# Performance work log

Measured on AMD Instinct MI355X. Metric: run time of the kernel, lower is better.

Reference implementation:

```python
import jax, jax.numpy as jnp
import numpy as np

B, N, C = 8, 1024, 768
H = 12
HD = C // H  # 64
SCALE = C ** (-0.5)  # NOTE: source scales by n_emb^-0.5, not head_dim^-0.5


def setup_inputs() -> dict:
    key = jax.random.key(0)
    k1, k2, k3 = jax.random.split(key, 3)
    x = jax.random.normal(k1, (B, N, C), dtype=jnp.float32)
    W_qkv = jax.random.normal(k2, (C, 3 * C), dtype=jnp.float32) * (C ** -0.5)
    b_qkv = jnp.zeros((3 * C,), dtype=jnp.float32)
    W_proj = jax.random.normal(k3, (C, C), dtype=jnp.float32) * (C ** -0.5)
    b_proj = jnp.zeros((C,), dtype=jnp.float32)
    return {"x": x, "W_qkv": W_qkv, "b_qkv": b_qkv, "W_proj": W_proj, "b_proj": b_proj}


def reference(x, W_qkv, b_qkv, W_proj, b_proj):
    # qkv projection: (B,N,3C) -> (3,B,H,N,HD)
    qkv = x @ W_qkv + b_qkv
    qkv = qkv.reshape(B, N, 3, H, HD).transpose(2, 0, 3, 1, 4)
    q, k, v = qkv[0], qkv[1], qkv[2]
    # scaled dot-product attention (full N x N, as in source)
    attn = jnp.einsum("bhnd,bhmd->bhnm", q, k) * SCALE
    attn = jax.nn.softmax(attn, axis=-1)
    out = jnp.einsum("bhnm,bhmd->bhnd", attn, v)
    out = out.transpose(0, 2, 1, 3).reshape(B, N, C)
    return out @ W_proj + b_proj
```

## Files before the change

kernel.cpp:

```cpp
#include <hip/hip_runtime.h>
#include <hip/hip_bf16.h>
#include <stdint.h>

#define Bb 8
#define Nn_ 1024
#define Cc_ 768
#define Hh 12
#define HDd 64
#define BHh 96
#define SCALE_F 0.03608439182435161f
#define CL2F (0.03608439182435161f * 1.4426950408889634f)
#define THRRAW (3.0f / CL2F)

typedef __attribute__((ext_vector_type(4))) float f32x4;
typedef __attribute__((ext_vector_type(8))) __bf16 bf16x8;

__device__ __forceinline__ unsigned short f2bf(float f) {
  uint32_t u = __builtin_bit_cast(uint32_t, f);
  uint32_t r = (u + 0x7fffu + ((u >> 16) & 1u)) >> 16;
  return (unsigned short)r;
}

__device__ __forceinline__ uint32_t cvtpk(float a, float b) {
  uint32_t r;
  asm("v_cvt_pk_bf16_f32 %0, %1, %2" : "=v"(r) : "v"(a), "v"(b));
  return r;
}

__device__ __forceinline__ f32x4 mfma16(bf16x8 a, bf16x8 b, f32x4 c) {
  return __builtin_amdgcn_mfma_f32_16x16x32_bf16(a, b, c, 0, 0, 0);
}

typedef const __attribute__((address_space(1))) uint32_t* gas1_t;
typedef __attribute__((address_space(3))) uint32_t* las3_t;
__device__ __forceinline__ void gl_lds16(const void* g, void* l) {
  __builtin_amdgcn_global_load_lds((gas1_t)g, (las3_t)l, 16, 0, 0);
}

#define VMCNT(n) asm volatile("s_waitcnt vmcnt(" #n ")" ::: "memory")
#define SBAR() __builtin_amdgcn_s_barrier()
#define SCHED_FENCE() __builtin_amdgcn_sched_barrier(0)

__global__ void k_cvt_x(const float* __restrict__ x, unsigned short* __restrict__ xb, int n4) {
  int i = blockIdx.x * blockDim.x + threadIdx.x;
  if (i >= n4) return;
  float4 v = ((const float4*)x)[i];
  ushort4 o;
  o.x = f2bf(v.x); o.y = f2bf(v.y); o.z = f2bf(v.z); o.w = f2bf(v.w);
  ((ushort4*)xb)[i] = o;
}

template <int R, int CC>
__global__ void k_transpose(const float* __restrict__ src, unsigned short* __restrict__ dst) {
  __shared__ unsigned short tile[64][65];
  int c0 = blockIdx.x * 64;
  int r0 = blockIdx.y * 64;
  int t = threadIdx.x;
#pragma unroll
  for (int i = 0; i < 16; ++i) {
    int idx = t + 256 * i;
    int r = idx >> 6, c = idx & 63;
    tile[r][c] = f2bf(src[(size_t)(r0 + r) * CC + c0 + c]);
  }
  __syncthreads();
#pragma unroll
  for (int i = 0; i < 16; ++i) {
    int idx = t + 256 * i;
    int a = idx >> 6, bq = idx & 63;
    dst[(size_t)(c0 + a) * R + r0 + bq] = tile[bq][a];
  }
}

__global__ __launch_bounds__(256) void k_transpose_v(const unsigned short* __restrict__ V,
                                                     unsigned short* __restrict__ Vt) {
  __shared__ unsigned short tile[64][72];
  int bh = blockIdx.y;
  int n0 = blockIdx.x * 64;
  int t = threadIdx.x;
  const unsigned short* src = V + ((size_t)bh * 1024 + n0) * 64;
#pragma unroll
  for (int i = 0; i < 4; ++i) {
    int idx = t + i * 256;
    int r = idx >> 4, c4 = idx & 15;
    ushort4 v = ((const ushort4*)src)[idx];
    tile[r][c4 * 4 + 0] = v.x; tile[r][c4 * 4 + 1] = v.y;
    tile[r][c4 * 4 + 2] = v.z; tile[r][c4 * 4 + 3] = v.w;
  }
  __syncthreads();
  unsigned short* dst = Vt + (size_t)bh * 64 * 1024 + n0;
#pragma unroll
  for (int i = 0; i < 4; ++i) {
    int idx = t + i * 256;
    int c = idx >> 4, n4 = idx & 15;
    ushort4 o;
    o.x = tile[n4 * 4 + 0][c]; o.y = tile[n4 * 4 + 1][c];
    o.z = tile[n4 * 4 + 2][c]; o.w = tile[n4 * 4 + 3][c];
    ((ushort4*)(dst + (size_t)c * 1024))[n4] = o;
  }
}

#define BM 128
#define BN 128

template <int EPI>
__global__ __launch_bounds__(256, 2) void k_gemm(
    const unsigned short* __restrict__ A, const unsigned short* __restrict__ Bt,
    const float* __restrict__ bias, float* __restrict__ out,
    unsigned short* __restrict__ Qb, unsigned short* __restrict__ Kb,
    unsigned short* __restrict__ Vb, int M, int Nw) {
  __shared__ char smem[2][32768];
  int t = threadIdx.x;
  int w = t >> 6, lane = t & 63;
  int g = lane >> 4, l15 = lane & 15;
  int m0 = blockIdx.x * BM;
  int n0 = blockIdx.y * BN;
  int wr = w >> 1, wc = w & 1;

  f32x4 acc[4][4] = {};

  int soff[4];
  const char* gA[4];
  const char* gB[4];
#pragma unroll
  for (int it = 0; it < 4; ++it) {
    int off = it * 4096 + t * 16;
    soff[it] = it * 4096 + w * 1024;
    int row = off >> 7;
    int sb = (off & 127) ^ ((row & 7) << 4);
    gA[it] = (const char*)A + (size_t)(m0 + row) * 1536 + sb;
    gB[it] = (const char*)Bt + (size_t)(n0 + row) * 1536 + sb;
  }

  auto STG = [&](int buf, int kt) {
    char* As = smem[buf];
    char* Bs = smem[buf] + 16384;
#pragma unroll
    for (int it = 0; it < 4; ++it) gl_lds16(gA[it] + kt * 128, As + soff[it]);
#pragma unroll
    for (int it = 0; it < 4; ++it) gl_lds16(gB[it] + kt * 128, Bs + soff[it]);
  };

  const char *pa[2][4], *pb[2][4];
#pragma unroll
  for (int ks = 0; ks < 2; ++ks) {
    int kb = ks * 64 + g * 16;
#pragma unroll
    for (int mi = 0; mi < 4; ++mi) {
      int rowA = wr * 64 + mi * 16 + l15;
      pa[ks][mi] = smem[0] + rowA * 128 + (kb ^ ((rowA & 7) << 4));
      int rowB = wc * 64 + mi * 16 + l15;
      pb[ks][mi] = smem[0] + 16384 + rowB * 128 + (kb ^ ((rowB & 7) << 4));
    }
  }

  auto CMP = [&](int off) {
    bf16x8 av[2][4], bv[2][4];
#pragma unroll
    for (int ks = 0; ks < 2; ++ks)
#pragma unroll
      for (int mi = 0; mi < 4; ++mi) {
        av[ks][mi] = *(const bf16x8*)(pa[ks][mi] + off);
        bv[ks][mi] = *(const bf16x8*)(pb[ks][mi] + off);
      }
#pragma unroll
    for (int ks = 0; ks < 2; ++ks)
#pragma unroll
      for (int mi = 0; mi < 4; ++mi)
#pragma unroll
        for (int ni = 0; ni < 4; ++ni)
          acc[mi][ni] = mfma16(av[ks][mi], bv[ks][ni], acc[mi][ni]);
  };

  STG(0, 0);
#pragma unroll
  for (int kt = 0; kt < 12; ++kt) {
    int cur = kt & 1;
    if (kt < 11) {
      STG(cur ^ 1, kt + 1);
      VMCNT(8);
    } else {
      VMCNT(0);
    }
    SBAR();
    SCHED_FENCE();
    CMP(cur * 32768);
    SCHED_FENCE();
    if (kt < 11) SBAR();
  }

#pragma unroll
  for (int mi = 0; mi < 4; ++mi) {
#pragma unroll
    for (int ni = 0; ni < 4; ++ni) {
      int col = n0 + wc * 64 + ni * 16 + l15;
      float bvs = bias[col];
#pragma unroll
      for (int j = 0; j < 4; ++j) {
        int row = m0 + wr * 64 + mi * 16 + g * 4 + j;
        float val = acc[mi][ni][j] + bvs;
        if constexpr (EPI == 0) {
          out[(size_t)row * Nw + col] = val;
        } else {
          int bI = row >> 10, n = row & 1023;
          int typ = col / 768, within = col % 768;
          int h = within >> 6, d = within & 63;
          int bh = bI * 12 + h;
          unsigned short bf = f2bf(val);
          unsigned short* dst = (typ == 0) ? Qb : (typ == 1) ? Kb : Vb;
          dst[((size_t)bh * 1024 + n) * 64 + d] = bf;
        }
      }
    }
  }
}

__global__ __launch_bounds__(256, 3) void k_attn(
    const unsigned short* __restrict__ Q, const unsigned short* __restrict__ K,
    const unsigned short* __restrict__ Vt, unsigned short* __restrict__ Oa) {
  __shared__ char smem[49152];
  char* Ks = smem;
  char* Ps = smem + 32768;
  int t = threadIdx.x, w = t >> 6, lane = t & 63;
  int g = lane >> 4, l15 = lane & 15;

  int fb = blockIdx.x;
  int bh = (fb & 7) * 12 + ((fb >> 3) % 12);
  int n0 = (fb / 96) * 128;
  int bI = bh / 12, h = bh % 12;
  char* Pw = Ps + w * 4096;

  bf16x8 qf[2][2];
  {
    const char* qbase = (const char*)Q + ((size_t)bh * 1024 + n0 + w * 32 + l15) * 128 + g * 16;
    qf[0][0] = *(const bf16x8*)(qbase);
    qf[0][1] = *(const bf16x8*)(qbase + 64);
    qf[1][0] = *(const bf16x8*)(qbase + 16 * 128);
    qf[1][1] = *(const bf16x8*)(qbase + 16 * 128 + 64);
  }

  f32x4 acc[2][4] = {};
  float mrun[2] = {-INFINITY, -INFINITY};
  float lrun[2] = {0.f, 0.f};

  const char* pK[2][4];
#pragma unroll
  for (int ks = 0; ks < 2; ++ks)
#pragma unroll
    for (int ff = 0; ff < 4; ++ff) {
      int row = ff * 16 + l15;
      pK[ks][ff] = Ks + row * 128 + ((ks * 64 + g * 16) ^ ((row & 7) << 4));
    }
  char* pPw[2][4];
  const char* pPr[2][2];
#pragma unroll
  for (int q = 0; q < 2; ++q) {
    int prow = q * 16 + l15, swz = (l15 & 7) << 4;
#pragma unroll
    for (int ff = 0; ff < 4; ++ff) pPw[q][ff] = Pw + prow * 128 + ((ff * 32 + g * 8) ^ swz);
#pragma unroll
    for (int ks = 0; ks < 2; ++ks) pPr[q][ks] = Pw + prow * 128 + ((ks * 64 + g * 16) ^ swz);
  }

  int o0 = t * 16, o1 = t * 16 + 4096;
  int r0 = o0 >> 7, r1 = o1 >> 7;
  int sb0 = (o0 & 127) ^ ((r0 & 7) << 4);
  int sb1 = (o1 & 127) ^ ((r1 & 7) << 4);
  const char* KgA = (const char*)K + (size_t)bh * 131072 + (size_t)r0 * 128 + sb0;
  const char* KgB = (const char*)K + (size_t)bh * 131072 + (size_t)r1 * 128 + sb1;
  const char* VgA = (const char*)Vt + (size_t)bh * 131072 + (size_t)r0 * 2048 + sb0;
  const char* VgB = (const char*)Vt + (size_t)bh * 131072 + (size_t)r1 * 2048 + sb1;

  auto STG = [&](int buf, int mt) {
    char* Kd = Ks + buf * 8192;
    char* Vd = Ks + 16384 + buf * 8192;
    gl_lds16(KgA + (size_t)mt * 8192, Kd + w * 1024);
    gl_lds16(KgB + (size_t)mt * 8192, Kd + 4096 + w * 1024);
    gl_lds16(VgA + (size_t)mt * 128, Vd + w * 1024);
    gl_lds16(VgB + (size_t)mt * 128, Vd + 4096 + w * 1024);
  };

  auto TILE = [&](int off) {
    f32x4 s[4][2] = {};
#pragma unroll
    for (int ks = 0; ks < 2; ++ks)
#pragma unroll
      for (int ff = 0; ff < 4; ++ff) {
        bf16x8 kv = *(const bf16x8*)(pK[ks][ff] + off);
        s[ff][0] = mfma16(kv, qf[0][ks], s[ff][0]);
        s[ff][1] = mfma16(kv, qf[1][ks], s[ff][1]);
      }

    float pmax[2];
#pragma unroll
    for (int q = 0; q < 2; ++q) {
      float a0 = fmaxf(fmaxf(s[0][q][0], s[0][q][1]), fmaxf(s[0][q][2], s[0][q][3]));
      float a1 = fmaxf(fmaxf(s[1][q][0], s[1][q][1]), fmaxf(s[1][q][2], s[1][q][3]));
      float a2 = fmaxf(fmaxf(s[2][q][0], s[2][q][1]), fmaxf(s[2][q][2], s[2][q][3]));
      float a3 = fmaxf(fmaxf(s[3][q][0], s[3][q][1]), fmaxf(s[3][q][2], s[3][q][3]));
      float pm = fmaxf(fmaxf(a0, a1), fmaxf(a2, a3));
      pm = fmaxf(pm, __shfl_xor(pm, 16, 64));
      pm = fmaxf(pm, __shfl_xor(pm, 32, 64));
      pmax[q] = pm;
    }

    bool upd = (pmax[0] > mrun[0] + THRRAW) || (pmax[1] > mrun[1] + THRRAW);
    if (__any(upd)) {
#pragma unroll
      for (int q = 0; q < 2; ++q) {
        float mnew = fmaxf(mrun[q], pmax[q]);
        float alpha = __builtin_amdgcn_exp2f((mrun[q] - mnew) * CL2F);
        mrun[q] = mnew;
        lrun[q] *= alpha;
#pragma unroll
        for (int j = 0; j < 4; ++j) {
          float aj = __shfl(alpha, g * 4 + j, 64);
          acc[q][0][j] *= aj; acc[q][1][j] *= aj;
          acc[q][2][j] *= aj; acc[q][3][j] *= aj;
        }
      }
    }

#pragma unroll
    for (int q = 0; q < 2; ++q) {
      float nm = -mrun[q] * CL2F;
      float rs = 0.f;
#pragma unroll
      for (int ff = 0; ff < 4; ++ff) {
        float p0 = __builtin_amdgcn_exp2f(fmaf(s[ff][q][0], CL2F, nm));
        float p1 = __builtin_amdgcn_exp2f(fmaf(s[ff][q][1], CL2F, nm));
        float p2 = __builtin_amdgcn_exp2f(fmaf(s[ff][q][2], CL2F, nm));
        float p3 = __builtin_amdgcn_exp2f(fmaf(s[ff][q][3], CL2F, nm));
        rs += (p0 + p1) + (p2 + p3);
        uint2 pk;
        pk.x = cvtpk(p0, p1);
        pk.y = cvtpk(p2, p3);
        *(uint2*)(pPw[q][ff]) = pk;
      }
      rs += __shfl_xor(rs, 16, 64);
      rs += __shfl_xor(rs, 32, 64);
      lrun[q] += rs;
    }

#pragma unroll
    for (int ks = 0; ks < 2; ++ks) {
      bf16x8 pa0 = *(const bf16x8*)(pPr[0][ks]);
      bf16x8 pa1 = *(const bf16x8*)(pPr[1][ks]);
#pragma unroll
      for (int fd = 0; fd < 4; ++fd) {
        bf16x8 vv = *(const bf16x8*)(pK[ks][fd] + 16384 + off);
        acc[0][fd] = mfma16(pa0, vv, acc[0][fd]);
        acc[1][fd] = mfma16(pa1, vv, acc[1][fd]);
      }
    }
  };

  STG(0, 0);
  for (int mt2 = 0; mt2 < 8; ++mt2) {
    STG(1, 2 * mt2 + 1);
    VMCNT(4);
    SBAR();
    SCHED_FENCE();
    TILE(0);
    SCHED_FENCE();
    SBAR();
    if (mt2 < 7) {
      STG(0, 2 * mt2 + 2);
      VMCNT(4);
    } else {
      VMCNT(0);
    }
    SBAR();
    SCHED_FENCE();
    TILE(8192);
    SCHED_FENCE();
    if (mt2 < 7) SBAR();
  }

#pragma unroll
  for (int q = 0; q < 2; ++q) {
#pragma unroll
    for (int j = 0; j < 4; ++j) {
      float lv = __shfl(lrun[q], g * 4 + j, 64);
      float inv = 1.0f / lv;
      int n = n0 + w * 32 + q * 16 + g * 4 + j;
      size_t rowb = ((size_t)bI * 1024 + n) * 768 + h * 64;
#pragma unroll
      for (int fd = 0; fd < 4; ++fd)
        Oa[rowb + fd * 16 + l15] = (unsigned short)(cvtpk(acc[q][fd][j] * inv, 0.f) & 0xffffu);
    }
  }
}

extern "C" void kernel_launch(void* const* d_in, const int* in_sizes, int n_in,
                              void* d_out, int out_size, void* d_ws, size_t ws_size,
                              hipStream_t stream) {
  const float* x = (const float*)d_in[0];
  const float* Wqkv = (const float*)d_in[1];
  const float* bqkv = (const float*)d_in[2];
  const float* Wproj = (const float*)d_in[3];
  const float* bproj = (const float*)d_in[4];
  float* out = (float*)d_out;

  char* ws = (char*)d_ws;
  unsigned short* xb  = (unsigned short*)(ws);
  unsigned short* wqt = (unsigned short*)(ws + 12582912);
  unsigned short* wpt = (unsigned short*)(ws + 16121856);
  unsigned short* Qb  = (unsigned short*)(ws + 17301504);
  unsigned short* Kb  = (unsigned short*)(ws + 29884416);
  unsigned short* Vtb = (unsigned short*)(ws + 42467328);
  unsigned short* Oa  = (unsigned short*)(ws + 55050240);
  unsigned short* Vb  = Oa;

  k_cvt_x<<<dim3(6144), dim3(256), 0, stream>>>(x, xb, (Bb * Nn_ * Cc_) / 4);
  k_transpose<768, 2304><<<dim3(36, 12), dim3(256), 0, stream>>>(Wqkv, wqt);
  k_transpose<768, 768><<<dim3(12, 12), dim3(256), 0, stream>>>(Wproj, wpt);
  k_gemm<1><<<dim3(64, 18), dim3(256), 0, stream>>>(xb, wqt, bqkv, nullptr, Qb, Kb, Vb,
                                                    8192, 2304);
  k_transpose_v<<<dim3(16, 96), dim3(256), 0, stream>>>(Vb, Vtb);
  k_attn<<<dim3(768), dim3(256), 0, stream>>>(Qb, Kb, Vtb, Oa);
  k_gemm<0><<<dim3(64, 6), dim3(256), 0, stream>>>(Oa, wpt, bproj, out, nullptr, nullptr, nullptr,
                                                   8192, 768);
}
```

Measured before the change: 114.1 us.

## Shrink GEMM K-tile, template M-tile, and cut attention LDS and reductions

The GEMM kernel switches from a 128-wide K step with XOR swizzle to a 64-wide K step without swizzle. The M tile becomes a template parameter, so the output projection uses 64-row tiles and launches twice as many blocks, and launch bounds rise to 4 blocks per CU. The attention kernel halves its per-wave P scratch by processing one query group at a time, which cuts LDS to 40KB for higher occupancy. It also defers the row-sum cross-lane reduction to the end, skips the max shuffle unless a rescale is needed, and adds setprio around the MFMA sections. Dropping the swizzle risks LDS bank conflicts, and the smaller K step doubles the number of barriers per GEMM.

```diff
diff --git a/kernel.cpp b/kernel.cpp
--- a/kernel.cpp
+++ b/kernel.cpp
@@ -99,104 +99,95 @@
   }
 }
 
-#define BM 128
-#define BN 128
-
-template <int EPI>
-__global__ __launch_bounds__(256, 2) void k_gemm(
+template <int EPI, int BMt>
+__global__ __launch_bounds__(256, 4) void k_gemm(
     const unsigned short* __restrict__ A, const unsigned short* __restrict__ Bt,
     const float* __restrict__ bias, float* __restrict__ out,
     unsigned short* __restrict__ Qb, unsigned short* __restrict__ Kb,
-    unsigned short* __restrict__ Vb, int M, int Nw) {
-  __shared__ char smem[2][32768];
+    unsigned short* __restrict__ Vb, int Nw) {
+  constexpr int WM = BMt / 2;
+  constexpr int MR = BMt / 32;
+  constexpr int AL = BMt / 64;
+  constexpr int BUFSZ = BMt * 64 + 8192;
+  constexpr int NLD = AL + 2;
+  __shared__ char smem[2 * BUFSZ];
   int t = threadIdx.x;
   int w = t >> 6, lane = t & 63;
   int g = lane >> 4, l15 = lane & 15;
-  int m0 = blockIdx.x * BM;
-  int n0 = blockIdx.y * BN;
+  int m0 = blockIdx.x * BMt;
+  int n0 = blockIdx.y * 128;
   int wr = w >> 1, wc = w & 1;
 
-  f32x4 acc[4][4] = {};
-
-  int soff[4];
-  const char* gA[4];
-  const char* gB[4];
-#pragma unroll
-  for (int it = 0; it < 4; ++it) {
-    int off = it * 4096 + t * 16;
-    soff[it] = it * 4096 + w * 1024;
-    int row = off >> 7;
-    int sb = (off & 127) ^ ((row & 7) << 4);
-    gA[it] = (const char*)A + (size_t)(m0 + row) * 1536 + sb;
-    gB[it] = (const char*)Bt + (size_t)(n0 + row) * 1536 + sb;
+  f32x4 acc[MR][4] = {};
+
+  const char* gA[AL];
+  const char* gB[2];
+  int sA[AL], sB[2];
+#pragma unroll
+  for (int it = 0; it < AL; ++it) {
+    int o = it * 4096 + t * 16;
+    gA[it] = (const char*)A + (size_t)(m0 + (o >> 6)) * 1536 + (o & 63);
+    sA[it] = it * 4096 + w * 1024;
+  }
+#pragma unroll
+  for (int it = 0; it < 2; ++it) {
+    int o = it * 4096 + t * 16;
+    gB[it] = (const char*)Bt + (size_t)(n0 + (o >> 6)) * 1536 + (o & 63);
+    sB[it] = BMt * 64 + it * 4096 + w * 1024;
   }
 
   auto STG = [&](int buf, int kt) {
-    char* As = smem[buf];
-    char* Bs = smem[buf] + 16384;
-#pragma unroll
-    for (int it = 0; it < 4; ++it) gl_lds16(gA[it] + kt * 128, As + soff[it]);
-#pragma unroll
-    for (int it = 0; it < 4; ++it) gl_lds16(gB[it] + kt * 128, Bs + soff[it]);
+    char* base = smem + buf * BUFSZ;
+#pragma unroll
+    for (int it = 0; it < AL; ++it) gl_lds16(gA[it] + kt * 64, base + sA[it]);
+#pragma unroll
+    for (int it = 0; it < 2; ++it) gl_lds16(gB[it] + kt * 64, base + sB[it]);
   };
 
-  const char *pa[2][4], *pb[2][4];
-#pragma unroll
-  for (int ks = 0; ks < 2; ++ks) {
-    int kb = ks * 64 + g * 16;
-#pragma unroll
-    for (int mi = 0; mi < 4; ++mi) {
-      int rowA = wr * 64 + mi * 16 + l15;
-      pa[ks][mi] = smem[0] + rowA * 128 + (kb ^ ((rowA & 7) << 4));
-      int rowB = wc * 64 + mi * 16 + l15;
-      pb[ks][mi] = smem[0] + 16384 + rowB * 128 + (kb ^ ((rowB & 7) << 4));
-    }
-  }
-
-  auto CMP = [&](int off) {
-    bf16x8 av[2][4], bv[2][4];
-#pragma unroll
-    for (int ks = 0; ks < 2; ++ks)
-#pragma unroll
-      for (int mi = 0; mi < 4; ++mi) {
-        av[ks][mi] = *(const bf16x8*)(pa[ks][mi] + off);
-        bv[ks][mi] = *(const bf16x8*)(pb[ks][mi] + off);
-      }
-#pragma unroll
-    for (int ks = 0; ks < 2; ++ks)
-#pragma unroll
-      for (int mi = 0; mi < 4; ++mi)
-#pragma unroll
-        for (int ni = 0; ni < 4; ++ni)
-          acc[mi][ni] = mfma16(av[ks][mi], bv[ks][ni], acc[mi][ni]);
-  };
+  const char* pa[MR];
+  const char* pb[4];
+#pragma unroll
+  for (int mi = 0; mi < MR; ++mi)
+    pa[mi] = smem + (wr * WM + mi * 16 + l15) * 64 + g * 16;
+#pragma unroll
+  for (int ni = 0; ni < 4; ++ni)
+    pb[ni] = smem + BMt * 64 + (wc * 64 + ni * 16 + l15) * 64 + g * 16;
 
   STG(0, 0);
 #pragma unroll
-  for (int kt = 0; kt < 12; ++kt) {
-    int cur = kt & 1;
-    if (kt < 11) {
-      STG(cur ^ 1, kt + 1);
-      VMCNT(8);
+  for (int kt = 0; kt < 24; ++kt) {
+    int off = (kt & 1) * BUFSZ;
+    if (kt < 23) {
+      STG((kt & 1) ^ 1, kt + 1);
+      if constexpr (NLD == 4) { VMCNT(4); } else { VMCNT(3); }
     } else {
       VMCNT(0);
     }
     SBAR();
     SCHED_FENCE();
-    CMP(cur * 32768);
-    SCHED_FENCE();
-    if (kt < 11) SBAR();
-  }
-
-#pragma unroll
-  for (int mi = 0; mi < 4; ++mi) {
+    bf16x8 av[MR], bv[4];
+#pragma unroll
+    for (int mi = 0; mi < MR; ++mi) av[mi] = *(const bf16x8*)(pa[mi] + off);
+#pragma unroll
+    for (int ni = 0; ni < 4; ++ni) bv[ni] = *(const bf16x8*)(pb[ni] + off);
+#pragma unroll
+    for (int mi = 0; mi < MR; ++mi)
+#pragma unroll
+      for (int ni = 0; ni < 4; ++ni)
+        acc[mi][ni] = mfma16(av[mi], bv[ni], acc[mi][ni]);
+    SCHED_FENCE();
+    if (kt < 23) SBAR();
+  }
+
+#pragma unroll
+  for (int mi = 0; mi < MR; ++mi) {
 #pragma unroll
     for (int ni = 0; ni < 4; ++ni) {
       int col = n0 + wc * 64 + ni * 16 + l15;
       float bvs = bias[col];
 #pragma unroll
       for (int j = 0; j < 4; ++j) {
-        int row = m0 + wr * 64 + mi * 16 + g * 4 + j;
+        int row = m0 + wr * WM + mi * 16 + g * 4 + j;
         float val = acc[mi][ni][j] + bvs;
         if constexpr (EPI == 0) {
           out[(size_t)row * Nw + col] = val;
@@ -214,12 +205,11 @@
   }
 }
 
-__global__ __launch_bounds__(256, 3) void k_attn(
+__global__ __launch_bounds__(256, 4) void k_attn(
     const unsigned short* __restrict__ Q, const unsigned short* __restrict__ K,
     const unsigned short* __restrict__ Vt, unsigned short* __restrict__ Oa) {
-  __shared__ char smem[49152];
+  __shared__ char smem[40960];
   char* Ks = smem;
-  char* Ps = smem + 32768;
   int t = threadIdx.x, w = t >> 6, lane = t & 63;
   int g = lane >> 4, l15 = lane & 15;
 
@@ -227,7 +217,7 @@
   int bh = (fb & 7) * 12 + ((fb >> 3) % 12);
   int n0 = (fb / 96) * 128;
   int bI = bh / 12, h = bh % 12;
-  char* Pw = Ps + w * 4096;
+  char* Pw = smem + 32768 + w * 2048;
 
   bf16x8 qf[2][2];
   {
@@ -243,22 +233,24 @@
   float lrun[2] = {0.f, 0.f};
 
   const char* pK[2][4];
+  const char* pV[2][4];
 #pragma unroll
   for (int ks = 0; ks < 2; ++ks)
 #pragma unroll
     for (int ff = 0; ff < 4; ++ff) {
       int row = ff * 16 + l15;
-      pK[ks][ff] = Ks + row * 128 + ((ks * 64 + g * 16) ^ ((row & 7) << 4));
-    }
-  char* pPw[2][4];
-  const char* pPr[2][2];
-#pragma unroll
-  for (int q = 0; q < 2; ++q) {
-    int prow = q * 16 + l15, swz = (l15 & 7) << 4;
-#pragma unroll
-    for (int ff = 0; ff < 4; ++ff) pPw[q][ff] = Pw + prow * 128 + ((ff * 32 + g * 8) ^ swz);
-#pragma unroll
-    for (int ks = 0; ks < 2; ++ks) pPr[q][ks] = Pw + prow * 128 + ((ks * 64 + g * 16) ^ swz);
+      int y = (ks * 64 + g * 16) ^ ((row & 7) << 4);
+      pK[ks][ff] = Ks + row * 128 + y;
+      pV[ks][ff] = smem + 16384 + row * 128 + y;
+    }
+  char* pPw[4];
+  const char* pPr[2];
+  {
+    int swz = (l15 & 7) << 4;
+#pragma unroll
+    for (int ff = 0; ff < 4; ++ff) pPw[ff] = Pw + l15 * 128 + ((ff * 32 + g * 8) ^ swz);
+#pragma unroll
+    for (int ks = 0; ks < 2; ++ks) pPr[ks] = Pw + l15 * 128 + ((ks * 64 + g * 16) ^ swz);
   }
 
   int o0 = t * 16, o1 = t * 16 + 4096;
@@ -272,7 +264,7 @@
 
   auto STG = [&](int buf, int mt) {
     char* Kd = Ks + buf * 8192;
-    char* Vd = Ks + 16384 + buf * 8192;
+    char* Vd = smem + 16384 + buf * 8192;
     gl_lds16(KgA + (size_t)mt * 8192, Kd + w * 1024);
     gl_lds16(KgB + (size_t)mt * 8192, Kd + 4096 + w * 1024);
     gl_lds16(VgA + (size_t)mt * 128, Vd + w * 1024);
@@ -281,6 +273,7 @@
 
   auto TILE = [&](int off) {
     f32x4 s[4][2] = {};
+    __builtin_amdgcn_s_setprio(1);
 #pragma unroll
     for (int ks = 0; ks < 2; ++ks)
 #pragma unroll
@@ -289,25 +282,25 @@
         s[ff][0] = mfma16(kv, qf[0][ks], s[ff][0]);
         s[ff][1] = mfma16(kv, qf[1][ks], s[ff][1]);
       }
-
-    float pmax[2];
+    __builtin_amdgcn_s_setprio(0);
+
+    float lmax[2];
 #pragma unroll
     for (int q = 0; q < 2; ++q) {
       float a0 = fmaxf(fmaxf(s[0][q][0], s[0][q][1]), fmaxf(s[0][q][2], s[0][q][3]));
       float a1 = fmaxf(fmaxf(s[1][q][0], s[1][q][1]), fmaxf(s[1][q][2], s[1][q][3]));
       float a2 = fmaxf(fmaxf(s[2][q][0], s[2][q][1]), fmaxf(s[2][q][2], s[2][q][3]));
       float a3 = fmaxf(fmaxf(s[3][q][0], s[3][q][1]), fmaxf(s[3][q][2], s[3][q][3]));
-      float pm = fmaxf(fmaxf(a0, a1), fmaxf(a2, a3));
-      pm = fmaxf(pm, __shfl_xor(pm, 16, 64));
-      pm = fmaxf(pm, __shfl_xor(pm, 32, 64));
-      pmax[q] = pm;
-    }
-
-    bool upd = (pmax[0] > mrun[0] + THRRAW) || (pmax[1] > mrun[1] + THRRAW);
+      lmax[q] = fmaxf(fmaxf(a0, a1), fmaxf(a2, a3));
+    }
+    bool upd = (lmax[0] > mrun[0] + THRRAW) || (lmax[1] > mrun[1] + THRRAW);
     if (__any(upd)) {
 #pragma unroll
       for (int q = 0; q < 2; ++q) {
-        float mnew = fmaxf(mrun[q], pmax[q]);
+        float pm = lmax[q];
+        pm = fmaxf(pm, __shfl_xor(pm, 16, 64));
+        pm = fmaxf(pm, __shfl_xor(pm, 32, 64));
+        float mnew = fmaxf(mrun[q], pm);
         float alpha = __builtin_amdgcn_exp2f((mrun[q] - mnew) * CL2F);
         mrun[q] = mnew;
         lrun[q] *= alpha;
@@ -334,23 +327,20 @@
         uint2 pk;
         pk.x = cvtpk(p0, p1);
         pk.y = cvtpk(p2, p3);
-        *(uint2*)(pPw[q][ff]) = pk;
+        *(uint2*)(pPw[ff]) = pk;
       }
-      rs += __shfl_xor(rs, 16, 64);
-      rs += __shfl_xor(rs, 32, 64);
       lrun[q] += rs;
-    }
-
-#pragma unroll
-    for (int ks = 0; ks < 2; ++ks) {
-      bf16x8 pa0 = *(const bf16x8*)(pPr[0][ks]);
-      bf16x8 pa1 = *(const bf16x8*)(pPr[1][ks]);
+      bf16x8 pa0 = *(const bf16x8*)(pPr[0]);
+      bf16x8 pa1 = *(const bf16x8*)(pPr[1]);
+      __builtin_amdgcn_s_setprio(1);
 #pragma unroll
       for (int fd = 0; fd < 4; ++fd) {
-        bf16x8 vv = *(const bf16x8*)(pK[ks][fd] + 16384 + off);
-        acc[0][fd] = mfma16(pa0, vv, acc[0][fd]);
-        acc[1][fd] = mfma16(pa1, vv, acc[1][fd]);
+        bf16x8 vv0 = *(const bf16x8*)(pV[0][fd] + off);
+        bf16x8 vv1 = *(const bf16x8*)(pV[1][fd] + off);
+        acc[q][fd] = mfma16(pa0, vv0, acc[q][fd]);
+        acc[q][fd] = mfma16(pa1, vv1, acc[q][fd]);
       }
+      __builtin_amdgcn_s_setprio(0);
     }
   };
 
@@ -376,6 +366,13 @@
     if (mt2 < 7) SBAR();
   }
 
+#pragma unroll
+  for (int q = 0; q < 2; ++q) {
+    float l = lrun[q];
+    l += __shfl_xor(l, 16, 64);
+    l += __shfl_xor(l, 32, 64);
+    lrun[q] = l;
+  }
 #pragma unroll
   for (int q = 0; q < 2; ++q) {
 #pragma unroll
@@ -414,10 +411,8 @@
   k_cvt_x<<<dim3(6144), dim3(256), 0, stream>>>(x, xb, (Bb * Nn_ * Cc_) / 4);
   k_transpose<768, 2304><<<dim3(36, 12), dim3(256), 0, stream>>>(Wqkv, wqt);
   k_transpose<768, 768><<<dim3(12, 12), dim3(256), 0, stream>>>(Wproj, wpt);
-  k_gemm<1><<<dim3(64, 18), dim3(256), 0, stream>>>(xb, wqt, bqkv, nullptr, Qb, Kb, Vb,
-                                                    8192, 2304);
+  k_gemm<1, 128><<<dim3(64, 18), dim3(256), 0, stream>>>(xb, wqt, bqkv, nullptr, Qb, Kb, Vb, 2304);
   k_transpose_v<<<dim3(16, 96), dim3(256), 0, stream>>>(Vb, Vtb);
   k_attn<<<dim3(768), dim3(256), 0, stream>>>(Qb, Kb, Vtb, Oa);
-  k_gemm<0><<<dim3(64, 6), dim3(256), 0, stream>>>(Oa, wpt, bproj, out, nullptr, nullptr, nullptr,
-                                                   8192, 768);
-}
+  k_gemm<0, 64><<<dim3(128, 6), dim3(256), 0, stream>>>(Oa, wpt, bproj, out, nullptr, nullptr, nullptr, 768);
+}
```

Measured after the change: 137.7 us. 1.21x slower.
